# Optimization experiments

Measured on AMD Instinct MI355X. Metric: run time of the kernel, lower is better.

The kernel has to match this reference:

```python
import jax, jax.numpy as jnp
import numpy as np

N_NODES = 100000
N_EDGES = 1600000
D_FEAT = 32
D_HID = 64
D_OUT = 64


def setup_inputs() -> dict:
    key = jax.random.key(0)
    ks = jax.random.split(key, 7)
    x = jax.random.normal(ks[0], (N_NODES, D_FEAT), dtype=jnp.float32)
    pos = jax.random.uniform(ks[1], (N_NODES, 3), dtype=jnp.float32) * 100.0
    # Fixed-size stand-in for radius_graph(pos, 5) output: (2, E) [source; target]
    edge_index = jax.random.randint(ks[2], (2, N_EDGES), 0, N_NODES, dtype=jnp.int64)
    d_in = D_FEAT + 3  # concat(x_j, pos_j - pos_i)
    W1 = jax.random.normal(ks[3], (d_in, D_HID), dtype=jnp.float32) / np.sqrt(d_in)
    b1 = jnp.zeros((D_HID,), dtype=jnp.float32)
    W2 = jax.random.normal(ks[4], (D_HID, D_OUT), dtype=jnp.float32) / np.sqrt(D_HID)
    b2 = jnp.zeros((D_OUT,), dtype=jnp.float32)
    return {"x": x, "pos": pos, "edge_index": edge_index,
            "W1": W1, "b1": b1, "W2": W2, "b2": b2}


def reference(x, pos, edge_index, W1, b1, W2, b2):
    n = x.shape[0]
    # PointNetConv default add_self_loops=True (radius_graph used loop=False)
    loops = jnp.arange(n, dtype=edge_index.dtype)
    src = jnp.concatenate([edge_index[0], loops])  # source j
    dst = jnp.concatenate([edge_index[1], loops])  # target i
    # gather: per-edge message input [E+N, d_feat+3]
    msg_in = jnp.concatenate([x[src], pos[src] - pos[dst]], axis=-1)
    # local_nn MLP
    h = jax.nn.relu(msg_in @ W1 + b1) @ W2 + b2
    # scatter: max-aggregate onto target nodes (PointConv aggr='max')
    out = jax.ops.segment_max(h, dst, num_segments=n)
    return out
```

## Files before the change

### kernel.cpp

```cpp
#include <hip/hip_runtime.h>
#include <hip/hip_bf16.h>
#include <math.h>

#define N_NODES 100000
#define N_EDGES 1600000
#define D_FEAT 32
#define D_HID 64
#define D_OUT 64
#define CAP 48
#define NPB 64
#define NBKT 1563
#define ECAP 1536
#define B1 256
#define E_PER_B1 6250
#define NB_NODE 1024

typedef short bf16x8 __attribute__((ext_vector_type(8)));
typedef float f32x4  __attribute__((ext_vector_type(4)));

__device__ inline unsigned short f2bf(float f) {
    unsigned u = __float_as_uint(f);
    u += 0x7fff + ((u >> 16) & 1);
    return (unsigned short)(u >> 16);
}
__device__ inline float bf2f(unsigned short h) {
    return __uint_as_float(((unsigned)h) << 16);
}

__global__ __launch_bounds__(256)
void node_kernel(const float* __restrict__ x,
                 const float* __restrict__ pos,
                 const float* __restrict__ W1,
                 const float* __restrict__ b1,
                 unsigned short* __restrict__ vb,
                 unsigned short* __restrict__ qb) {
    const int lane = threadIdx.x & 63;
    const int wid  = (blockIdx.x * blockDim.x + threadIdx.x) >> 6;
    const int nw   = (NB_NODE * 256) >> 6;

    float w[D_FEAT + 3];
#pragma unroll
    for (int f = 0; f < D_FEAT + 3; ++f)
        w[f] = W1[f * D_HID + lane];
    const float bb = b1[lane];

    for (int node = wid; node < N_NODES; node += nw) {
        const float* xr = x + (size_t)node * D_FEAT;
        float acc = bb;
#pragma unroll
        for (int f = 0; f < D_FEAT; ++f)
            acc = fmaf(xr[f], w[f], acc);

        const float* pr = pos + (size_t)node * 3;
        float qa = 0.0f;
#pragma unroll
        for (int p = 0; p < 3; ++p)
            qa = fmaf(pr[p], w[D_FEAT + p], qa);

        vb[(size_t)node * D_HID + lane] = f2bf(acc + qa);
        qb[(size_t)node * D_HID + lane] = f2bf(qa);
    }
}

__global__ __launch_bounds__(1024)
void bin_kernel(const int* __restrict__ src,
                const int* __restrict__ dst,
                int* __restrict__ gcnt,
                unsigned int* __restrict__ coarse) {
    __shared__ int hist[NBKT];
    const int tid = threadIdx.x;
    const int e0 = blockIdx.x * E_PER_B1;
    const int e1 = e0 + E_PER_B1;

    for (int b = tid; b < NBKT; b += 1024) hist[b] = 0;
    __syncthreads();

    for (int e = e0 + tid; e < e1; e += 1024)
        atomicAdd(&hist[dst[e] >> 6], 1);
    __syncthreads();

    for (int b = tid; b < NBKT; b += 1024) {
        int c = hist[b];
        hist[b] = (c > 0) ? atomicAdd(&gcnt[b], c) : 0;
    }
    __syncthreads();

    for (int e = e0 + tid; e < e1; e += 1024) {
        int d = dst[e], s = src[e];
        int b = d >> 6;
        int pos = atomicAdd(&hist[b], 1);
        if (pos < ECAP)
            coarse[(size_t)b * ECAP + pos] = ((unsigned)s << 6) | (unsigned)(d & 63);
    }
}

__global__ __launch_bounds__(256)
void agg_kernel(const unsigned short* __restrict__ vb,
                const unsigned short* __restrict__ qb,
                const float* __restrict__ W2,
                const float* __restrict__ b2,
                const int* __restrict__ gcnt,
                const unsigned int* __restrict__ coarse,
                float* __restrict__ out) {
    __shared__ int lcnt[NPB];
    __shared__ int lslots[NPB][CAP];

    const int tid  = threadIdx.x;
    const int lane = tid & 63;
    const int wave = tid >> 6;
    const int quad = lane >> 4;
    const int mrow = lane & 15;
    const int bkt  = blockIdx.x;
    const int nbase = bkt << 6;

    bf16x8 bfrag[4][2];
#pragma unroll
    for (int t = 0; t < 4; ++t)
#pragma unroll
        for (int kh = 0; kh < 2; ++kh) {
            bf16x8 f;
#pragma unroll
            for (int j = 0; j < 8; ++j)
                f[j] = (short)f2bf(W2[(kh * 32 + quad * 8 + j) * D_OUT + t * 16 + mrow]);
            bfrag[t][kh] = f;
        }
    float bias[4];
#pragma unroll
    for (int t = 0; t < 4; ++t) bias[t] = b2[t * 16 + mrow];

    int E_b = gcnt[bkt];
    if (E_b > ECAP) E_b = ECAP;
    for (int i = tid; i < NPB; i += 256) lcnt[i] = 0;
    __syncthreads();
    for (int i = tid; i < E_b; i += 256) {
        unsigned enc = coarse[(size_t)bkt * ECAP + i];
        int local = (int)(enc & 63u);
        int s     = (int)(enc >> 6);
        int p = atomicAdd(&lcnt[local], 1);
        if (p < CAP) lslots[local][p] = s;
    }
    __syncthreads();

    for (int ln = wave; ln < NPB; ln += 4) {
        const int node = nbase + ln;
        if (node >= N_NODES) break;

        float qf[2][8];
#pragma unroll
        for (int kh = 0; kh < 2; ++kh) {
            bf16x8 qv = *(const bf16x8*)(qb + (size_t)node * D_HID + kh * 32 + quad * 8);
#pragma unroll
            for (int j = 0; j < 8; ++j) qf[kh][j] = bf2f((unsigned short)qv[j]);
        }

        int deg = lcnt[ln];
        if (deg > CAP) deg = CAP;
        const int rows = deg + 1;
        const int nbat = (rows + 15) >> 4;

        float rmax[4][4];
#pragma unroll
        for (int t = 0; t < 4; ++t)
#pragma unroll
            for (int r = 0; r < 4; ++r) rmax[t][r] = -INFINITY;

        for (int b = 0; b < nbat; ++b) {
            int idx = b * 16 + mrow;
            int idxc = (idx < CAP) ? idx : (CAP - 1);
            int s = (idx < deg) ? lslots[ln][idxc] : node;

            bf16x8 afrag[2];
#pragma unroll
            for (int kh = 0; kh < 2; ++kh) {
                bf16x8 vv = *(const bf16x8*)(vb + (size_t)s * D_HID + kh * 32 + quad * 8);
                bf16x8 a;
#pragma unroll
                for (int j = 0; j < 8; j += 2) {
                    float h0 = fmaxf(bf2f((unsigned short)vv[j])     - qf[kh][j],     0.0f);
                    float h1 = fmaxf(bf2f((unsigned short)vv[j + 1]) - qf[kh][j + 1], 0.0f);
                    __hip_bfloat162 p2 = __float22bfloat162_rn(make_float2(h0, h1));
                    a[j]     = (short)__bfloat16_as_ushort(p2.x);
                    a[j + 1] = (short)__bfloat16_as_ushort(p2.y);
                }
                afrag[kh] = a;
            }

            f32x4 acc[4];
#pragma unroll
            for (int t = 0; t < 4; ++t) {
                acc[t] = (f32x4){0.f, 0.f, 0.f, 0.f};
                acc[t] = __builtin_amdgcn_mfma_f32_16x16x32_bf16(afrag[0], bfrag[t][0], acc[t], 0, 0, 0);
                acc[t] = __builtin_amdgcn_mfma_f32_16x16x32_bf16(afrag[1], bfrag[t][1], acc[t], 0, 0, 0);
#pragma unroll
                for (int r = 0; r < 4; ++r)
                    rmax[t][r] = fmaxf(rmax[t][r], acc[t][r]);
            }
        }

        float fin[4];
#pragma unroll
        for (int t = 0; t < 4; ++t) {
            float m = fmaxf(fmaxf(rmax[t][0], rmax[t][1]), fmaxf(rmax[t][2], rmax[t][3]));
            m = fmaxf(m, __shfl_xor(m, 16, 64));
            m = fmaxf(m, __shfl_xor(m, 32, 64));
            fin[t] = m + bias[t];
        }
        float r = (quad == 0) ? fin[0] : (quad == 1) ? fin[1] : (quad == 2) ? fin[2] : fin[3];
        out[(size_t)node * D_OUT + lane] = r;
    }
}

extern "C" void kernel_launch(void* const* d_in, const int* in_sizes, int n_in,
                              void* d_out, int out_size, void* d_ws, size_t ws_size,
                              hipStream_t stream) {
    const float* x   = (const float*)d_in[0];
    const float* pos = (const float*)d_in[1];
    const int*   ei  = (const int*)d_in[2];
    const float* W1  = (const float*)d_in[3];
    const float* b1  = (const float*)d_in[4];
    const float* W2  = (const float*)d_in[5];
    const float* b2  = (const float*)d_in[6];
    float* out = (float*)d_out;

    char* ws = (char*)d_ws;
    unsigned short* vb   = (unsigned short*)ws;
    unsigned short* qb   = (unsigned short*)(ws + 12800000);
    int*            gcnt = (int*)(ws + 25600000);
    unsigned int* coarse = (unsigned int*)(ws + 25610240);

    const int* src = ei;
    const int* dst = ei + N_EDGES;

    hipMemsetAsync(gcnt, 0, NBKT * sizeof(int), stream);
    hipLaunchKernelGGL(bin_kernel, dim3(B1), dim3(1024), 0, stream,
                       src, dst, gcnt, coarse);
    hipLaunchKernelGGL(node_kernel, dim3(NB_NODE), dim3(256), 0, stream,
                       x, pos, W1, b1, vb, qb);
    hipLaunchKernelGGL(agg_kernel, dim3(NBKT), dim3(256), 0, stream,
                       vb, qb, W2, b2, gcnt, coarse, out);
}
```

Before: 211.9 us.

## Fuse binning and node precompute into one launch, use fp16 packed math

Merges the edge-binning and per-node W1 precompute kernels into a single launch whose block ranges take different roles, so the two independent phases run concurrently and one launch is saved. Switches the intermediate storage and the MFMA inputs from bf16 to fp16, so the subtract-and-ReLU runs as packed half vector ops without float round trips. Doubles the aggregation block to 512 threads (8 waves per bucket). fp16 has a narrower range than bf16, so precision and overflow behaviour change.

```diff
diff --git a/kernel.cpp b/kernel.cpp
--- a/kernel.cpp
+++ b/kernel.cpp
@@ -1,5 +1,4 @@
 #include <hip/hip_runtime.h>
-#include <hip/hip_bf16.h>
 #include <math.h>
 
 #define N_NODES 100000
@@ -13,88 +12,88 @@
 #define ECAP 1536
 #define B1 256
 #define E_PER_B1 6250
-#define NB_NODE 1024
-
-typedef short bf16x8 __attribute__((ext_vector_type(8)));
+#define NBN 256
+#define AGG_T 512
+
+typedef _Float16 half8 __attribute__((ext_vector_type(8)));
 typedef float f32x4  __attribute__((ext_vector_type(4)));
 
-__device__ inline unsigned short f2bf(float f) {
-    unsigned u = __float_as_uint(f);
-    u += 0x7fff + ((u >> 16) & 1);
-    return (unsigned short)(u >> 16);
-}
-__device__ inline float bf2f(unsigned short h) {
-    return __uint_as_float(((unsigned)h) << 16);
-}
-
-__global__ __launch_bounds__(256)
-void node_kernel(const float* __restrict__ x,
+__device__ inline half8 h8_subrelu(half8 v, half8 q) {
+    half8 z = {};
+    return __builtin_elementwise_max(v - q, z);
+}
+
+__global__ __launch_bounds__(1024)
+void prep_kernel(const int* __restrict__ src,
+                 const int* __restrict__ dst,
+                 int* __restrict__ gcnt,
+                 unsigned int* __restrict__ coarse,
+                 const float* __restrict__ x,
                  const float* __restrict__ pos,
                  const float* __restrict__ W1,
                  const float* __restrict__ b1,
                  unsigned short* __restrict__ vb,
                  unsigned short* __restrict__ qb) {
-    const int lane = threadIdx.x & 63;
-    const int wid  = (blockIdx.x * blockDim.x + threadIdx.x) >> 6;
-    const int nw   = (NB_NODE * 256) >> 6;
-
-    float w[D_FEAT + 3];
-#pragma unroll
-    for (int f = 0; f < D_FEAT + 3; ++f)
-        w[f] = W1[f * D_HID + lane];
-    const float bb = b1[lane];
-
-    for (int node = wid; node < N_NODES; node += nw) {
-        const float* xr = x + (size_t)node * D_FEAT;
-        float acc = bb;
-#pragma unroll
-        for (int f = 0; f < D_FEAT; ++f)
-            acc = fmaf(xr[f], w[f], acc);
-
-        const float* pr = pos + (size_t)node * 3;
-        float qa = 0.0f;
-#pragma unroll
-        for (int p = 0; p < 3; ++p)
-            qa = fmaf(pr[p], w[D_FEAT + p], qa);
-
-        vb[(size_t)node * D_HID + lane] = f2bf(acc + qa);
-        qb[(size_t)node * D_HID + lane] = f2bf(qa);
-    }
-}
-
-__global__ __launch_bounds__(1024)
-void bin_kernel(const int* __restrict__ src,
-                const int* __restrict__ dst,
-                int* __restrict__ gcnt,
-                unsigned int* __restrict__ coarse) {
     __shared__ int hist[NBKT];
     const int tid = threadIdx.x;
-    const int e0 = blockIdx.x * E_PER_B1;
-    const int e1 = e0 + E_PER_B1;
-
-    for (int b = tid; b < NBKT; b += 1024) hist[b] = 0;
-    __syncthreads();
-
-    for (int e = e0 + tid; e < e1; e += 1024)
-        atomicAdd(&hist[dst[e] >> 6], 1);
-    __syncthreads();
-
-    for (int b = tid; b < NBKT; b += 1024) {
-        int c = hist[b];
-        hist[b] = (c > 0) ? atomicAdd(&gcnt[b], c) : 0;
+
+    if (blockIdx.x < B1) {
+        const int e0 = blockIdx.x * E_PER_B1;
+        const int e1 = e0 + E_PER_B1;
+
+        for (int b = tid; b < NBKT; b += 1024) hist[b] = 0;
+        __syncthreads();
+
+        for (int e = e0 + tid; e < e1; e += 1024)
+            atomicAdd(&hist[dst[e] >> 6], 1);
+        __syncthreads();
+
+        for (int b = tid; b < NBKT; b += 1024) {
+            int c = hist[b];
+            hist[b] = (c > 0) ? atomicAdd(&gcnt[b], c) : 0;
+        }
+        __syncthreads();
+
+        for (int e = e0 + tid; e < e1; e += 1024) {
+            int d = dst[e], s = src[e];
+            int b = d >> 6;
+            int p = atomicAdd(&hist[b], 1);
+            if (p < ECAP)
+                coarse[(size_t)b * ECAP + p] = ((unsigned)s << 6) | (unsigned)(d & 63);
+        }
+    } else {
+        const int lane = tid & 63;
+        const int wid  = (((blockIdx.x - B1) * 1024) + tid) >> 6;
+        const int nw   = (NBN * 1024) >> 6;
+
+        float w[D_FEAT + 3];
+#pragma unroll
+        for (int f = 0; f < D_FEAT + 3; ++f)
+            w[f] = W1[f * D_HID + lane];
+        const float bb = b1[lane];
+
+        for (int node = wid; node < N_NODES; node += nw) {
+            const float* xr = x + (size_t)node * D_FEAT;
+            float acc = bb;
+#pragma unroll
+            for (int f = 0; f < D_FEAT; ++f)
+                acc = fmaf(xr[f], w[f], acc);
+
+            const float* pr = pos + (size_t)node * 3;
+            float qa = 0.0f;
+#pragma unroll
+            for (int p = 0; p < 3; ++p)
+                qa = fmaf(pr[p], w[D_FEAT + p], qa);
+
+            vb[(size_t)node * D_HID + lane] =
+                __builtin_bit_cast(unsigned short, (_Float16)(acc + qa));
+            qb[(size_t)node * D_HID + lane] =
+                __builtin_bit_cast(unsigned short, (_Float16)qa);
+        }
     }
-    __syncthreads();
-
-    for (int e = e0 + tid; e < e1; e += 1024) {
-        int d = dst[e], s = src[e];
-        int b = d >> 6;
-        int pos = atomicAdd(&hist[b], 1);
-        if (pos < ECAP)
-            coarse[(size_t)b * ECAP + pos] = ((unsigned)s << 6) | (unsigned)(d & 63);
-    }
-}
-
-__global__ __launch_bounds__(256)
+}
+
+__global__ __launch_bounds__(AGG_T)
 void agg_kernel(const unsigned short* __restrict__ vb,
                 const unsigned short* __restrict__ qb,
                 const float* __restrict__ W2,
@@ -113,15 +112,15 @@
     const int bkt  = blockIdx.x;
     const int nbase = bkt << 6;
 
-    bf16x8 bfrag[4][2];
+    half8 bfrag[4][2];
 #pragma unroll
     for (int t = 0; t < 4; ++t)
 #pragma unroll
         for (int kh = 0; kh < 2; ++kh) {
-            bf16x8 f;
+            half8 f;
 #pragma unroll
             for (int j = 0; j < 8; ++j)
-                f[j] = (short)f2bf(W2[(kh * 32 + quad * 8 + j) * D_OUT + t * 16 + mrow]);
+                f[j] = (_Float16)W2[(kh * 32 + quad * 8 + j) * D_OUT + t * 16 + mrow];
             bfrag[t][kh] = f;
         }
     float bias[4];
@@ -130,9 +129,9 @@
 
     int E_b = gcnt[bkt];
     if (E_b > ECAP) E_b = ECAP;
-    for (int i = tid; i < NPB; i += 256) lcnt[i] = 0;
+    for (int i = tid; i < NPB; i += AGG_T) lcnt[i] = 0;
     __syncthreads();
-    for (int i = tid; i < E_b; i += 256) {
+    for (int i = tid; i < E_b; i += AGG_T) {
         unsigned enc = coarse[(size_t)bkt * ECAP + i];
         int local = (int)(enc & 63u);
         int s     = (int)(enc >> 6);
@@ -141,17 +140,12 @@
     }
     __syncthreads();
 
-    for (int ln = wave; ln < NPB; ln += 4) {
+    for (int ln = wave; ln < NPB; ln += 8) {
         const int node = nbase + ln;
         if (node >= N_NODES) break;
 
-        float qf[2][8];
-#pragma unroll
-        for (int kh = 0; kh < 2; ++kh) {
-            bf16x8 qv = *(const bf16x8*)(qb + (size_t)node * D_HID + kh * 32 + quad * 8);
-#pragma unroll
-            for (int j = 0; j < 8; ++j) qf[kh][j] = bf2f((unsigned short)qv[j]);
-        }
+        const half8 q0 = *(const half8*)(qb + (size_t)node * D_HID + quad * 8);
+        const half8 q1 = *(const half8*)(qb + (size_t)node * D_HID + 32 + quad * 8);
 
         int deg = lcnt[ln];
         if (deg > CAP) deg = CAP;
@@ -169,31 +163,20 @@
             int idxc = (idx < CAP) ? idx : (CAP - 1);
             int s = (idx < deg) ? lslots[ln][idxc] : node;
 
-            bf16x8 afrag[2];
-#pragma unroll
-            for (int kh = 0; kh < 2; ++kh) {
-                bf16x8 vv = *(const bf16x8*)(vb + (size_t)s * D_HID + kh * 32 + quad * 8);
-                bf16x8 a;
-#pragma unroll
-                for (int j = 0; j < 8; j += 2) {
-                    float h0 = fmaxf(bf2f((unsigned short)vv[j])     - qf[kh][j],     0.0f);
-                    float h1 = fmaxf(bf2f((unsigned short)vv[j + 1]) - qf[kh][j + 1], 0.0f);
-                    __hip_bfloat162 p2 = __float22bfloat162_rn(make_float2(h0, h1));
-                    a[j]     = (short)__bfloat16_as_ushort(p2.x);
-                    a[j + 1] = (short)__bfloat16_as_ushort(p2.y);
-                }
-                afrag[kh] = a;
-            }
-
-            f32x4 acc[4];
+            const half8 v0 = *(const half8*)(vb + (size_t)s * D_HID + quad * 8);
+            const half8 v1 = *(const half8*)(vb + (size_t)s * D_HID + 32 + quad * 8);
+
+            half8 a0 = h8_subrelu(v0, q0);
+            half8 a1 = h8_subrelu(v1, q1);
+
 #pragma unroll
             for (int t = 0; t < 4; ++t) {
-                acc[t] = (f32x4){0.f, 0.f, 0.f, 0.f};
-                acc[t] = __builtin_amdgcn_mfma_f32_16x16x32_bf16(afrag[0], bfrag[t][0], acc[t], 0, 0, 0);
-                acc[t] = __builtin_amdgcn_mfma_f32_16x16x32_bf16(afrag[1], bfrag[t][1], acc[t], 0, 0, 0);
+                f32x4 acc = (f32x4){0.f, 0.f, 0.f, 0.f};
+                acc = __builtin_amdgcn_mfma_f32_16x16x32_f16(a0, bfrag[t][0], acc, 0, 0, 0);
+                acc = __builtin_amdgcn_mfma_f32_16x16x32_f16(a1, bfrag[t][1], acc, 0, 0, 0);
 #pragma unroll
                 for (int r = 0; r < 4; ++r)
-                    rmax[t][r] = fmaxf(rmax[t][r], acc[t][r]);
+                    rmax[t][r] = fmaxf(rmax[t][r], acc[r]);
             }
         }
 
@@ -232,10 +215,8 @@
     const int* dst = ei + N_EDGES;
 
     hipMemsetAsync(gcnt, 0, NBKT * sizeof(int), stream);
-    hipLaunchKernelGGL(bin_kernel, dim3(B1), dim3(1024), 0, stream,
-                       src, dst, gcnt, coarse);
-    hipLaunchKernelGGL(node_kernel, dim3(NB_NODE), dim3(256), 0, stream,
-                       x, pos, W1, b1, vb, qb);
-    hipLaunchKernelGGL(agg_kernel, dim3(NBKT), dim3(256), 0, stream,
+    hipLaunchKernelGGL(prep_kernel, dim3(B1 + NBN), dim3(1024), 0, stream,
+                       src, dst, gcnt, coarse, x, pos, W1, b1, vb, qb);
+    hipLaunchKernelGGL(agg_kernel, dim3(NBKT), dim3(AGG_T), 0, stream,
                        vb, qb, W2, b2, gcnt, coarse, out);
 }
```

Measured after the change: 249.0 us. 17.5% more time.
